# Kernel tuning notes

Hardware: AMD Instinct MI355X
Metric: run time of the kernel (lower is better)

The kernel has to match this reference:

```python
import jax, jax.numpy as jnp
import numpy as np

N_NODES = 50000
N_EDGES = 800000
D = 128
RRELU_SLOPE = (1.0 / 8.0 + 1.0 / 3.0) / 2.0  # eval-mode RReLU = leaky relu with mean slope 11/48


def setup_inputs() -> dict:
    key = jax.random.key(0)
    ks = jax.random.split(key, 10)
    s = 1.0 / np.sqrt(D)
    return {
        "node_feats": jax.random.normal(ks[0], (N_NODES, D), dtype=jnp.float32),
        "edge_feats": jax.random.normal(ks[1], (N_EDGES, D), dtype=jnp.float32),
        "src": jax.random.randint(ks[2], (N_EDGES,), 0, N_NODES, dtype=jnp.int32),
        "dst": jax.random.randint(ks[3], (N_EDGES,), 0, N_NODES, dtype=jnp.int32),
        "Wn0": jax.random.uniform(ks[4], (D, D), jnp.float32, -s, s),
        "Ws0": jax.random.uniform(ks[5], (D, D), jnp.float32, -s, s),
        "Wi0": jax.random.uniform(ks[6], (D, D), jnp.float32, -s, s),
        "Wn1": jax.random.uniform(ks[7], (D, D), jnp.float32, -s, s),
        "Ws1": jax.random.uniform(ks[8], (D, D), jnp.float32, -s, s),
        "Wi1": jax.random.uniform(ks[9], (D, D), jnp.float32, -s, s),
    }


def _layer(h, edge_feats, src, dst, deg, iso, Wn, Ws, Wi, num_nodes):
    # per-edge message: neigh_linear(src_h + edge_h)
    msg = (h[src] + edge_feats) @ Wn.T  # [E, H]
    # mean aggregate to destination; nodes with no in-edges get 0 (DGL semantics)
    agg = jax.ops.segment_sum(msg, dst, num_segments=num_nodes)
    agg = agg / jnp.maximum(deg, 1.0)[:, None]
    # self-loop message, replaced by isolated-node message where in_degree == 0
    self_msg = jnp.where(iso[:, None], h @ Wi.T, h @ Ws.T)
    x = agg + self_msg
    # RReLU in eval mode = leaky relu with slope (lower+upper)/2
    return jnp.where(x >= 0, x, RRELU_SLOPE * x)


def reference(node_feats, edge_feats, src, dst, Wn0, Ws0, Wi0, Wn1, Ws1, Wi1):
    num_nodes = node_feats.shape[0]
    deg = jax.ops.segment_sum(
        jnp.ones(src.shape[0], dtype=node_feats.dtype), dst, num_segments=num_nodes
    )
    iso = deg == 0
    h = _layer(node_feats, edge_feats, src, dst, deg, iso, Wn0, Ws0, Wi0, num_nodes)
    h = _layer(h, edge_feats, src, dst, deg, iso, Wn1, Ws1, Wi1, num_nodes)
    return h
```

## Files before the change

### kernel.cpp

```cpp
#include <hip/hip_runtime.h>
#include <hip/hip_bf16.h>

#define N_NODES 50000
#define N_EDGES 800000
#define D 128
#define D2 64

static constexpr float SLOPE = 11.0f / 48.0f;

typedef __attribute__((ext_vector_type(8))) short bf16x8;
typedef __attribute__((ext_vector_type(4))) float f32x4;
typedef __attribute__((ext_vector_type(2))) unsigned int u32x2;
typedef __attribute__((ext_vector_type(4))) unsigned int u32x4;

__device__ __forceinline__ float bf_lo(unsigned int v) { return __uint_as_float(v << 16); }
__device__ __forceinline__ float bf_hi(unsigned int v) { return __uint_as_float(v & 0xffff0000u); }

__device__ __forceinline__ unsigned short f2bf(float x) {
    __hip_bfloat16 b = __float2bfloat16(x);
    return *(unsigned short*)&b;
}

__device__ __forceinline__ unsigned int pack_bf2(float lo, float hi) {
    return ((unsigned int)f2bf(hi) << 16) | (unsigned int)f2bf(lo);
}


__global__ void k_cvt_nf(const f32x4* __restrict__ in, u32x4* __restrict__ out) {
    int i = blockIdx.x * 256 + threadIdx.x;
    if (i >= N_NODES * D / 8) return;
    f32x4 lo = in[2 * i];
    f32x4 hi = in[2 * i + 1];
    u32x4 o;
    o.x = pack_bf2(lo[0], lo[1]);
    o.y = pack_bf2(lo[2], lo[3]);
    o.z = pack_bf2(hi[0], hi[1]);
    o.w = pack_bf2(hi[2], hi[3]);
    out[i] = o;
}

__global__ void k_cvt_w(const float* __restrict__ Wn0, const float* __restrict__ Ws0,
                        const float* __restrict__ Wn1, const float* __restrict__ Ws1,
                        unsigned int* __restrict__ out) {
    int i = blockIdx.x * 256 + threadIdx.x;
    int m = i >> 11;
    int j = i & 2047;
    const float* W = (m == 0) ? Wn0 : (m == 1) ? Ws0 : (m == 2) ? Wn1 : Ws1;
    f32x4 lo = ((const f32x4*)W)[2 * j];
    f32x4 hi = ((const f32x4*)W)[2 * j + 1];
    u32x4 o;
    o.x = pack_bf2(lo[0], lo[1]);
    o.y = pack_bf2(lo[2], lo[3]);
    o.z = pack_bf2(hi[0], hi[1]);
    o.w = pack_bf2(hi[2], hi[3]);
    *(u32x4*)(out + (size_t)m * 8192 + 4 * j) = o;
}


__global__ void k_count(const int* __restrict__ dst, int* __restrict__ deg) {
    int e = blockIdx.x * 256 + threadIdx.x;
    if (e < N_EDGES) atomicAdd(&deg[dst[e]], 1);
}

__global__ void k_scan1(const int* __restrict__ deg, int* __restrict__ offs,
                        int* __restrict__ part) {
    __shared__ int sm[256];
    int t = threadIdx.x;
    int i = blockIdx.x * 256 + t;
    int v = (i < N_NODES) ? deg[i] : 0;
    int orig = v;
    sm[t] = v;
    __syncthreads();
    for (int off = 1; off < 256; off <<= 1) {
        int x = (t >= off) ? sm[t - off] : 0;
        __syncthreads();
        sm[t] += x;
        __syncthreads();
    }
    if (i < N_NODES) offs[i] = sm[t] - orig;
    if (t == 255) part[blockIdx.x] = sm[t];
}

__global__ void k_scan2(int* __restrict__ part, int nb) {
    __shared__ int sm[256];
    int t = threadIdx.x;
    int v = (t < nb) ? part[t] : 0;
    int orig = v;
    sm[t] = v;
    __syncthreads();
    for (int off = 1; off < 256; off <<= 1) {
        int x = (t >= off) ? sm[t - off] : 0;
        __syncthreads();
        sm[t] += x;
        __syncthreads();
    }
    if (t < nb) part[t] = sm[t] - orig;
}

__global__ void k_scan3(int* __restrict__ offs, const int* __restrict__ part) {
    int i = blockIdx.x * 256 + threadIdx.x;
    if (i < N_NODES) offs[i] += part[blockIdx.x];
}

__global__ void k_fill(const int* __restrict__ src, const int* __restrict__ dst,
                       const int* __restrict__ offs, int* __restrict__ cur,
                       int2* __restrict__ csr) {
    int e = blockIdx.x * 256 + threadIdx.x;
    if (e < N_EDGES) {
        int d = dst[e];
        int p = offs[d] + atomicAdd(&cur[d], 1);
        csr[p] = make_int2(src[e], e);
    }
}

__global__ void k_iso(const int* __restrict__ deg, int* __restrict__ isolist,
                      int* __restrict__ niso) {
    int i = blockIdx.x * 256 + threadIdx.x;
    if (i < N_NODES && deg[i] == 0) {
        int p = atomicAdd(niso, 1);
        isolist[p] = i;
    }
}


__global__ void k_agg_ef(const unsigned int* __restrict__ nfb,
                         const f32x4* __restrict__ ef,
                         const int2* __restrict__ csr,
                         const int* __restrict__ offs, const int* __restrict__ deg,
                         unsigned int* __restrict__ efsum,
                         unsigned int* __restrict__ pre) {
    int node = blockIdx.x * 4 + (threadIdx.x >> 6);
    if (node >= N_NODES) return;
    int lane = threadIdx.x & 63;
    int half = lane >> 5;
    int c = lane & 31;
    int start = offs[node];
    int cnt = deg[node];
    f32x4 ae = {0.f, 0.f, 0.f, 0.f};
    f32x4 ah = {0.f, 0.f, 0.f, 0.f};
#pragma unroll 2
    for (int k = half; k < cnt; k += 2) {
        int2 se = csr[start + k];
        f32x4 ev = ef[(size_t)se.y * 32 + c];
        u32x2 hv = *(const u32x2*)(nfb + (size_t)se.x * D2 + 2 * c);
        ae[0] += ev[0];
        ae[1] += ev[1];
        ae[2] += ev[2];
        ae[3] += ev[3];
        ah[0] += bf_lo(hv.x);
        ah[1] += bf_hi(hv.x);
        ah[2] += bf_lo(hv.y);
        ah[3] += bf_hi(hv.y);
    }
#pragma unroll
    for (int i = 0; i < 4; ++i) {
        ae[i] += __shfl_xor(ae[i], 32);
        ah[i] += __shfl_xor(ah[i], 32);
    }
    float inv = 1.0f / fmaxf((float)cnt, 1.0f);
    if (half == 0) {
        u32x2 eo;
        eo.x = pack_bf2(ae[0], ae[1]);
        eo.y = pack_bf2(ae[2], ae[3]);
        *(u32x2*)(efsum + (size_t)node * D2 + 2 * c) = eo;
    } else {
        u32x2 po;
        po.x = pack_bf2((ah[0] + ae[0]) * inv, (ah[1] + ae[1]) * inv);
        po.y = pack_bf2((ah[2] + ae[2]) * inv, (ah[3] + ae[3]) * inv);
        *(u32x2*)(pre + (size_t)node * D2 + 2 * c) = po;
    }
}


__global__ void k_agg2(const unsigned int* __restrict__ h,
                       const int2* __restrict__ csr,
                       const int* __restrict__ offs, const int* __restrict__ deg,
                       const unsigned int* __restrict__ efsum,
                       unsigned int* __restrict__ pre) {
    int node = blockIdx.x * 4 + (threadIdx.x >> 6);
    if (node >= N_NODES) return;
    int lane = threadIdx.x & 63;
    int q = lane >> 4;
    int g = lane & 15;
    int start = offs[node];
    int cnt = deg[node];
    float a[8] = {0.f, 0.f, 0.f, 0.f, 0.f, 0.f, 0.f, 0.f};
#pragma unroll 2
    for (int k = q; k < cnt; k += 4) {
        int2 se = csr[start + k];
        u32x4 hv = *(const u32x4*)(h + (size_t)se.x * D2 + 4 * g);
        a[0] += bf_lo(hv.x);
        a[1] += bf_hi(hv.x);
        a[2] += bf_lo(hv.y);
        a[3] += bf_hi(hv.y);
        a[4] += bf_lo(hv.z);
        a[5] += bf_hi(hv.z);
        a[6] += bf_lo(hv.w);
        a[7] += bf_hi(hv.w);
    }
#pragma unroll
    for (int i = 0; i < 8; ++i) {
        a[i] += __shfl_xor(a[i], 16);
        a[i] += __shfl_xor(a[i], 32);
    }
    if (q == 0) {
        u32x4 es = *(const u32x4*)(efsum + (size_t)node * D2 + 4 * g);
        float inv = 1.0f / fmaxf((float)cnt, 1.0f);
        float r0 = (a[0] + bf_lo(es.x)) * inv;
        float r1 = (a[1] + bf_hi(es.x)) * inv;
        float r2 = (a[2] + bf_lo(es.y)) * inv;
        float r3 = (a[3] + bf_hi(es.y)) * inv;
        float r4 = (a[4] + bf_lo(es.z)) * inv;
        float r5 = (a[5] + bf_hi(es.z)) * inv;
        float r6 = (a[6] + bf_lo(es.w)) * inv;
        float r7 = (a[7] + bf_hi(es.w)) * inv;
        u32x4 o;
        o.x = pack_bf2(r0, r1);
        o.y = pack_bf2(r2, r3);
        o.z = pack_bf2(r4, r5);
        o.w = pack_bf2(r6, r7);
        *(u32x4*)(pre + (size_t)node * D2 + 4 * g) = o;
    }
}


template <int OUT_F32>
__global__ void k_gemm(const unsigned short* __restrict__ A1,
                       const unsigned short* __restrict__ A2,
                       const unsigned short* __restrict__ W1,
                       const unsigned short* __restrict__ W2,
                       void* __restrict__ outv) {
    int wave = threadIdx.x >> 6;
    int lane = threadIdx.x & 63;
    int quad = lane >> 4;
    int r16 = lane & 15;
    int m0 = (blockIdx.x * 4 + wave) * 32;

    f32x4 acc[2][8];
#pragma unroll
    for (int mt = 0; mt < 2; ++mt)
#pragma unroll
        for (int nt = 0; nt < 8; ++nt) acc[mt][nt] = (f32x4){0.f, 0.f, 0.f, 0.f};

    int rowA0 = min(m0 + r16, N_NODES - 1);
    int rowA1 = min(m0 + 16 + r16, N_NODES - 1);

#pragma unroll
    for (int ks = 0; ks < 8; ++ks) {
        int koff = (ks & 3) * 32 + quad * 8;
        const unsigned short* Asrc = (ks < 4) ? A1 : A2;
        bf16x8 a0 = *(const bf16x8*)(Asrc + (size_t)rowA0 * D + koff);
        bf16x8 a1 = *(const bf16x8*)(Asrc + (size_t)rowA1 * D + koff);
        const unsigned short* Wsrc = (ks < 4) ? W1 : W2;
#pragma unroll
        for (int nt = 0; nt < 8; ++nt) {
            bf16x8 b = *(const bf16x8*)(Wsrc + (size_t)(nt * 16 + r16) * D + koff);
            acc[0][nt] = __builtin_amdgcn_mfma_f32_16x16x32_bf16(a0, b, acc[0][nt], 0, 0, 0);
            acc[1][nt] = __builtin_amdgcn_mfma_f32_16x16x32_bf16(a1, b, acc[1][nt], 0, 0, 0);
        }
    }

#pragma unroll
    for (int mt = 0; mt < 2; ++mt) {
#pragma unroll
        for (int r = 0; r < 4; ++r) {
            int row = m0 + mt * 16 + quad * 4 + r;
            if (row < N_NODES) {
#pragma unroll
                for (int nt = 0; nt < 8; ++nt) {
                    float x = acc[mt][nt][r];
                    x = (x >= 0.f) ? x : x * SLOPE;
                    if (OUT_F32)
                        ((float*)outv)[(size_t)row * D + nt * 16 + r16] = x;
                    else
                        ((unsigned short*)outv)[(size_t)row * D + nt * 16 + r16] = f2bf(x);
                }
            }
        }
    }
}


__global__ void k_fixup1(const unsigned int* __restrict__ nfb,
                         const float* __restrict__ Wi,
                         const int* __restrict__ isolist, const int* __restrict__ niso,
                         unsigned short* __restrict__ out) {
    int w = blockIdx.x * 4 + (threadIdx.x >> 6);
    int lane = threadIdx.x & 63;
    int n = *niso;
    for (int t = w; t < n; t += gridDim.x * 4) {
        int node = isolist[t];
        const unsigned int* hrow = nfb + (size_t)node * D2;
        float a0 = 0.f, a1 = 0.f;
        for (int ku = 0; ku < D2; ++ku) {
            unsigned int v = hrow[ku];
            float h0 = bf_lo(v), h1 = bf_hi(v);
            a0 += h0 * Wi[(size_t)lane * D + 2 * ku] + h1 * Wi[(size_t)lane * D + 2 * ku + 1];
            a1 += h0 * Wi[(size_t)(lane + 64) * D + 2 * ku] +
                  h1 * Wi[(size_t)(lane + 64) * D + 2 * ku + 1];
        }
        a0 = (a0 >= 0.f) ? a0 : a0 * SLOPE;
        a1 = (a1 >= 0.f) ? a1 : a1 * SLOPE;
        out[(size_t)node * D + lane] = f2bf(a0);
        out[(size_t)node * D + lane + 64] = f2bf(a1);
    }
}

__global__ void k_fixup2(const unsigned short* __restrict__ h,
                         const float* __restrict__ Wi,
                         const int* __restrict__ isolist, const int* __restrict__ niso,
                         float* __restrict__ out) {
    int w = blockIdx.x * 4 + (threadIdx.x >> 6);
    int lane = threadIdx.x & 63;
    int n = *niso;
    for (int t = w; t < n; t += gridDim.x * 4) {
        int node = isolist[t];
        const unsigned short* hrow = h + (size_t)node * D;
        float a0 = 0.f, a1 = 0.f;
        for (int k = 0; k < D; ++k) {
            float hk = __uint_as_float(((unsigned int)hrow[k]) << 16);
            a0 += hk * Wi[(size_t)lane * D + k];
            a1 += hk * Wi[(size_t)(lane + 64) * D + k];
        }
        a0 = (a0 >= 0.f) ? a0 : a0 * SLOPE;
        a1 = (a1 >= 0.f) ? a1 : a1 * SLOPE;
        out[(size_t)node * D + lane] = a0;
        out[(size_t)node * D + lane + 64] = a1;
    }
}


extern "C" void kernel_launch(void* const* d_in, const int* in_sizes, int n_in,
                              void* d_out, int out_size, void* d_ws, size_t ws_size,
                              hipStream_t stream) {
    const float* node_feats = (const float*)d_in[0];
    const float* edge_feats = (const float*)d_in[1];
    const int* src = (const int*)d_in[2];
    const int* dst = (const int*)d_in[3];
    const float* Wn0 = (const float*)d_in[4];
    const float* Ws0 = (const float*)d_in[5];
    const float* Wi0 = (const float*)d_in[6];
    const float* Wn1 = (const float*)d_in[7];
    const float* Ws1 = (const float*)d_in[8];
    const float* Wi1 = (const float*)d_in[9];

    char* ws = (char*)d_ws;
    size_t o = 0;
    auto alloc = [&](size_t bytes) -> char* {
        char* p = ws + o;
        o += (bytes + 255) & ~size_t(255);
        return p;
    };
    int* deg = (int*)alloc((size_t)N_NODES * 4);
    int* cur = (int*)alloc((size_t)N_NODES * 4);
    int* niso = (int*)alloc(256);
    int* offs = (int*)alloc((size_t)N_NODES * 4);
    int* part = (int*)alloc(1024);
    int* isolist = (int*)alloc((size_t)N_NODES * 4);
    int2* csr = (int2*)alloc((size_t)N_EDGES * 8);
    unsigned int* efsum = (unsigned int*)alloc((size_t)N_NODES * D * 2);
    unsigned int* pre = (unsigned int*)alloc((size_t)N_NODES * D * 2);
    unsigned int* h1 = (unsigned int*)alloc((size_t)N_NODES * D * 2);
    unsigned int* nfb = (unsigned int*)alloc((size_t)N_NODES * D * 2);
    unsigned int* wbf = (unsigned int*)alloc(4 * 8192 * 4);

    hipMemsetAsync(deg, 0, 2 * (((size_t)N_NODES * 4 + 255) & ~size_t(255)) + 256, stream);

    int ebl = (N_EDGES + 255) / 256;
    int nbl = (N_NODES + 255) / 256;
    int nwb = (N_NODES + 3) / 4;
    int gbl = (N_NODES + 127) / 128;

    k_cvt_nf<<<(N_NODES * D / 8 + 255) / 256, 256, 0, stream>>>((const f32x4*)node_feats,
                                                                (u32x4*)nfb);
    k_cvt_w<<<32, 256, 0, stream>>>(Wn0, Ws0, Wn1, Ws1, wbf);
    k_count<<<ebl, 256, 0, stream>>>(dst, deg);
    k_scan1<<<nbl, 256, 0, stream>>>(deg, offs, part);
    k_scan2<<<1, 256, 0, stream>>>(part, nbl);
    k_scan3<<<nbl, 256, 0, stream>>>(offs, part);
    k_fill<<<ebl, 256, 0, stream>>>(src, dst, offs, cur, csr);
    k_iso<<<nbl, 256, 0, stream>>>(deg, isolist, niso);

    const unsigned short* Wn0b = (const unsigned short*)(wbf + 0 * 8192);
    const unsigned short* Ws0b = (const unsigned short*)(wbf + 1 * 8192);
    const unsigned short* Wn1b = (const unsigned short*)(wbf + 2 * 8192);
    const unsigned short* Ws1b = (const unsigned short*)(wbf + 3 * 8192);

    k_agg_ef<<<nwb, 256, 0, stream>>>(nfb, (const f32x4*)edge_feats, csr, offs, deg, efsum, pre);
    k_gemm<0><<<gbl, 256, 0, stream>>>((const unsigned short*)pre, (const unsigned short*)nfb,
                                       Wn0b, Ws0b, (void*)h1);
    k_fixup1<<<32, 256, 0, stream>>>(nfb, Wi0, isolist, niso, (unsigned short*)h1);

    k_agg2<<<nwb, 256, 0, stream>>>(h1, csr, offs, deg, efsum, pre);
    k_gemm<1><<<gbl, 256, 0, stream>>>((const unsigned short*)pre, (const unsigned short*)h1,
                                       Wn1b, Ws1b, d_out);
    k_fixup2<<<32, 256, 0, stream>>>((const unsigned short*)h1, Wi1, isolist, niso, (float*)d_out);
}
```

Measured before the change: 757.0 us.

## Merge setup kernels, widen gather lanes, and halve GEMM wave tile

Merges the node-feature and weight conversions into one launch and folds the isolated-node list building into the first scan kernel. The scan now writes absolute offsets into the cursor array, so the fill kernel no longer reads offs and the memset shrinks. The edge-aggregation kernels are regrouped so each lane issues wider vector loads over more edges at once (4 and 8 edges in parallel per wave). The GEMM drops from 32 to 16 rows per wave and doubles the block count, trading B-fragment reuse for more parallelism.

```diff
diff --git a/kernel.cpp b/kernel.cpp
--- a/kernel.cpp
+++ b/kernel.cpp
@@ -26,34 +26,37 @@
 }
 
 
-__global__ void k_cvt_nf(const f32x4* __restrict__ in, u32x4* __restrict__ out) {
+__global__ void k_cvt(const f32x4* __restrict__ nf, const float* __restrict__ Wn0,
+                      const float* __restrict__ Ws0, const float* __restrict__ Wn1,
+                      const float* __restrict__ Ws1, u32x4* __restrict__ nfb,
+                      unsigned int* __restrict__ wbf) {
     int i = blockIdx.x * 256 + threadIdx.x;
-    if (i >= N_NODES * D / 8) return;
-    f32x4 lo = in[2 * i];
-    f32x4 hi = in[2 * i + 1];
-    u32x4 o;
-    o.x = pack_bf2(lo[0], lo[1]);
-    o.y = pack_bf2(lo[2], lo[3]);
-    o.z = pack_bf2(hi[0], hi[1]);
-    o.w = pack_bf2(hi[2], hi[3]);
-    out[i] = o;
-}
-
-__global__ void k_cvt_w(const float* __restrict__ Wn0, const float* __restrict__ Ws0,
-                        const float* __restrict__ Wn1, const float* __restrict__ Ws1,
-                        unsigned int* __restrict__ out) {
-    int i = blockIdx.x * 256 + threadIdx.x;
-    int m = i >> 11;
-    int j = i & 2047;
-    const float* W = (m == 0) ? Wn0 : (m == 1) ? Ws0 : (m == 2) ? Wn1 : Ws1;
-    f32x4 lo = ((const f32x4*)W)[2 * j];
-    f32x4 hi = ((const f32x4*)W)[2 * j + 1];
-    u32x4 o;
-    o.x = pack_bf2(lo[0], lo[1]);
-    o.y = pack_bf2(lo[2], lo[3]);
-    o.z = pack_bf2(hi[0], hi[1]);
-    o.w = pack_bf2(hi[2], hi[3]);
-    *(u32x4*)(out + (size_t)m * 8192 + 4 * j) = o;
+    const int NNF = N_NODES * D / 8;
+    if (i < NNF) {
+        f32x4 lo = nf[2 * i];
+        f32x4 hi = nf[2 * i + 1];
+        u32x4 o;
+        o.x = pack_bf2(lo[0], lo[1]);
+        o.y = pack_bf2(lo[2], lo[3]);
+        o.z = pack_bf2(hi[0], hi[1]);
+        o.w = pack_bf2(hi[2], hi[3]);
+        nfb[i] = o;
+    } else {
+        int j = i - NNF;
+        if (j < 8192) {
+            int m = j >> 11;
+            int t = j & 2047;
+            const float* W = (m == 0) ? Wn0 : (m == 1) ? Ws0 : (m == 2) ? Wn1 : Ws1;
+            f32x4 lo = ((const f32x4*)W)[2 * t];
+            f32x4 hi = ((const f32x4*)W)[2 * t + 1];
+            u32x4 o;
+            o.x = pack_bf2(lo[0], lo[1]);
+            o.y = pack_bf2(lo[2], lo[3]);
+            o.z = pack_bf2(hi[0], hi[1]);
+            o.w = pack_bf2(hi[2], hi[3]);
+            *(u32x4*)(wbf + (size_t)m * 8192 + 4 * t) = o;
+        }
+    }
 }
 
 
@@ -63,12 +66,17 @@
 }
 
 __global__ void k_scan1(const int* __restrict__ deg, int* __restrict__ offs,
-                        int* __restrict__ part) {
+                        int* __restrict__ part, int* __restrict__ isolist,
+                        int* __restrict__ niso) {
     __shared__ int sm[256];
     int t = threadIdx.x;
     int i = blockIdx.x * 256 + t;
     int v = (i < N_NODES) ? deg[i] : 0;
     int orig = v;
+    if (i < N_NODES && orig == 0) {
+        int p = atomicAdd(niso, 1);
+        isolist[p] = i;
+    }
     sm[t] = v;
     __syncthreads();
     for (int off = 1; off < 256; off <<= 1) {
@@ -97,28 +105,22 @@
     if (t < nb) part[t] = sm[t] - orig;
 }
 
-__global__ void k_scan3(int* __restrict__ offs, const int* __restrict__ part) {
+__global__ void k_scan3(int* __restrict__ offs, const int* __restrict__ part,
+                        int* __restrict__ cur) {
     int i = blockIdx.x * 256 + threadIdx.x;
-    if (i < N_NODES) offs[i] += part[blockIdx.x];
+    if (i < N_NODES) {
+        int v = offs[i] + part[blockIdx.x];
+        offs[i] = v;
+        cur[i] = v;
+    }
 }
 
 __global__ void k_fill(const int* __restrict__ src, const int* __restrict__ dst,
-                       const int* __restrict__ offs, int* __restrict__ cur,
-                       int2* __restrict__ csr) {
+                       int* __restrict__ cur, int2* __restrict__ csr) {
     int e = blockIdx.x * 256 + threadIdx.x;
     if (e < N_EDGES) {
-        int d = dst[e];
-        int p = offs[d] + atomicAdd(&cur[d], 1);
+        int p = atomicAdd(&cur[dst[e]], 1);
         csr[p] = make_int2(src[e], e);
-    }
-}
-
-__global__ void k_iso(const int* __restrict__ deg, int* __restrict__ isolist,
-                      int* __restrict__ niso) {
-    int i = blockIdx.x * 256 + threadIdx.x;
-    if (i < N_NODES && deg[i] == 0) {
-        int p = atomicAdd(niso, 1);
-        isolist[p] = i;
     }
 }
 
@@ -132,42 +134,57 @@
     int node = blockIdx.x * 4 + (threadIdx.x >> 6);
     if (node >= N_NODES) return;
     int lane = threadIdx.x & 63;
-    int half = lane >> 5;
-    int c = lane & 31;
+    int q = lane >> 4;
+    int g = lane & 15;
     int start = offs[node];
     int cnt = deg[node];
-    f32x4 ae = {0.f, 0.f, 0.f, 0.f};
-    f32x4 ah = {0.f, 0.f, 0.f, 0.f};
+    float ae[8] = {0.f, 0.f, 0.f, 0.f, 0.f, 0.f, 0.f, 0.f};
+    float ah[8] = {0.f, 0.f, 0.f, 0.f, 0.f, 0.f, 0.f, 0.f};
 #pragma unroll 2
-    for (int k = half; k < cnt; k += 2) {
+    for (int k = q; k < cnt; k += 4) {
         int2 se = csr[start + k];
-        f32x4 ev = ef[(size_t)se.y * 32 + c];
-        u32x2 hv = *(const u32x2*)(nfb + (size_t)se.x * D2 + 2 * c);
-        ae[0] += ev[0];
-        ae[1] += ev[1];
-        ae[2] += ev[2];
-        ae[3] += ev[3];
+        f32x4 e0 = ef[(size_t)se.y * 32 + 2 * g];
+        f32x4 e1 = ef[(size_t)se.y * 32 + 2 * g + 1];
+        u32x4 hv = *(const u32x4*)(nfb + (size_t)se.x * D2 + 4 * g);
+        ae[0] += e0[0];
+        ae[1] += e0[1];
+        ae[2] += e0[2];
+        ae[3] += e0[3];
+        ae[4] += e1[0];
+        ae[5] += e1[1];
+        ae[6] += e1[2];
+        ae[7] += e1[3];
         ah[0] += bf_lo(hv.x);
         ah[1] += bf_hi(hv.x);
         ah[2] += bf_lo(hv.y);
         ah[3] += bf_hi(hv.y);
-    }
-#pragma unroll
-    for (int i = 0; i < 4; ++i) {
+        ah[4] += bf_lo(hv.z);
+        ah[5] += bf_hi(hv.z);
+        ah[6] += bf_lo(hv.w);
+        ah[7] += bf_hi(hv.w);
+    }
+#pragma unroll
+    for (int i = 0; i < 8; ++i) {
+        ae[i] += __shfl_xor(ae[i], 16);
         ae[i] += __shfl_xor(ae[i], 32);
+        ah[i] += __shfl_xor(ah[i], 16);
         ah[i] += __shfl_xor(ah[i], 32);
     }
     float inv = 1.0f / fmaxf((float)cnt, 1.0f);
-    if (half == 0) {
-        u32x2 eo;
+    if (q == 0) {
+        u32x4 eo;
         eo.x = pack_bf2(ae[0], ae[1]);
         eo.y = pack_bf2(ae[2], ae[3]);
-        *(u32x2*)(efsum + (size_t)node * D2 + 2 * c) = eo;
-    } else {
-        u32x2 po;
+        eo.z = pack_bf2(ae[4], ae[5]);
+        eo.w = pack_bf2(ae[6], ae[7]);
+        *(u32x4*)(efsum + (size_t)node * D2 + 4 * g) = eo;
+    } else if (q == 1) {
+        u32x4 po;
         po.x = pack_bf2((ah[0] + ae[0]) * inv, (ah[1] + ae[1]) * inv);
         po.y = pack_bf2((ah[2] + ae[2]) * inv, (ah[3] + ae[3]) * inv);
-        *(u32x2*)(pre + (size_t)node * D2 + 2 * c) = po;
+        po.z = pack_bf2((ah[4] + ae[4]) * inv, (ah[5] + ae[5]) * inv);
+        po.w = pack_bf2((ah[6] + ae[6]) * inv, (ah[7] + ae[7]) * inv);
+        *(u32x4*)(pre + (size_t)node * D2 + 4 * g) = po;
     }
 }
 
@@ -180,46 +197,56 @@
     int node = blockIdx.x * 4 + (threadIdx.x >> 6);
     if (node >= N_NODES) return;
     int lane = threadIdx.x & 63;
-    int q = lane >> 4;
-    int g = lane & 15;
+    int e = lane >> 3;
+    int g = lane & 7;
     int start = offs[node];
     int cnt = deg[node];
-    float a[8] = {0.f, 0.f, 0.f, 0.f, 0.f, 0.f, 0.f, 0.f};
+    float a[16];
+#pragma unroll
+    for (int i = 0; i < 16; ++i) a[i] = 0.f;
 #pragma unroll 2
-    for (int k = q; k < cnt; k += 4) {
+    for (int k = e; k < cnt; k += 8) {
         int2 se = csr[start + k];
-        u32x4 hv = *(const u32x4*)(h + (size_t)se.x * D2 + 4 * g);
-        a[0] += bf_lo(hv.x);
-        a[1] += bf_hi(hv.x);
-        a[2] += bf_lo(hv.y);
-        a[3] += bf_hi(hv.y);
-        a[4] += bf_lo(hv.z);
-        a[5] += bf_hi(hv.z);
-        a[6] += bf_lo(hv.w);
-        a[7] += bf_hi(hv.w);
-    }
-#pragma unroll
-    for (int i = 0; i < 8; ++i) {
+        u32x4 h0 = *(const u32x4*)(h + (size_t)se.x * D2 + 8 * g);
+        u32x4 h1v = *(const u32x4*)(h + (size_t)se.x * D2 + 8 * g + 4);
+        a[0] += bf_lo(h0.x);
+        a[1] += bf_hi(h0.x);
+        a[2] += bf_lo(h0.y);
+        a[3] += bf_hi(h0.y);
+        a[4] += bf_lo(h0.z);
+        a[5] += bf_hi(h0.z);
+        a[6] += bf_lo(h0.w);
+        a[7] += bf_hi(h0.w);
+        a[8] += bf_lo(h1v.x);
+        a[9] += bf_hi(h1v.x);
+        a[10] += bf_lo(h1v.y);
+        a[11] += bf_hi(h1v.y);
+        a[12] += bf_lo(h1v.z);
+        a[13] += bf_hi(h1v.z);
+        a[14] += bf_lo(h1v.w);
+        a[15] += bf_hi(h1v.w);
+    }
+#pragma unroll
+    for (int i = 0; i < 16; ++i) {
+        a[i] += __shfl_xor(a[i], 8);
         a[i] += __shfl_xor(a[i], 16);
         a[i] += __shfl_xor(a[i], 32);
     }
-    if (q == 0) {
-        u32x4 es = *(const u32x4*)(efsum + (size_t)node * D2 + 4 * g);
+    if (e == 0) {
+        u32x4 e0 = *(const u32x4*)(efsum + (size_t)node * D2 + 8 * g);
+        u32x4 e1 = *(const u32x4*)(efsum + (size_t)node * D2 + 8 * g + 4);
         float inv = 1.0f / fmaxf((float)cnt, 1.0f);
-        float r0 = (a[0] + bf_lo(es.x)) * inv;
-        float r1 = (a[1] + bf_hi(es.x)) * inv;
-        float r2 = (a[2] + bf_lo(es.y)) * inv;
-        float r3 = (a[3] + bf_hi(es.y)) * inv;
-        float r4 = (a[4] + bf_lo(es.z)) * inv;
-        float r5 = (a[5] + bf_hi(es.z)) * inv;
-        float r6 = (a[6] + bf_lo(es.w)) * inv;
-        float r7 = (a[7] + bf_hi(es.w)) * inv;
-        u32x4 o;
-        o.x = pack_bf2(r0, r1);
-        o.y = pack_bf2(r2, r3);
-        o.z = pack_bf2(r4, r5);
-        o.w = pack_bf2(r6, r7);
-        *(u32x4*)(pre + (size_t)node * D2 + 4 * g) = o;
+        u32x4 o0, o1;
+        o0.x = pack_bf2((a[0] + bf_lo(e0.x)) * inv, (a[1] + bf_hi(e0.x)) * inv);
+        o0.y = pack_bf2((a[2] + bf_lo(e0.y)) * inv, (a[3] + bf_hi(e0.y)) * inv);
+        o0.z = pack_bf2((a[4] + bf_lo(e0.z)) * inv, (a[5] + bf_hi(e0.z)) * inv);
+        o0.w = pack_bf2((a[6] + bf_lo(e0.w)) * inv, (a[7] + bf_hi(e0.w)) * inv);
+        o1.x = pack_bf2((a[8] + bf_lo(e1.x)) * inv, (a[9] + bf_hi(e1.x)) * inv);
+        o1.y = pack_bf2((a[10] + bf_lo(e1.y)) * inv, (a[11] + bf_hi(e1.y)) * inv);
+        o1.z = pack_bf2((a[12] + bf_lo(e1.z)) * inv, (a[13] + bf_hi(e1.z)) * inv);
+        o1.w = pack_bf2((a[14] + bf_lo(e1.w)) * inv, (a[15] + bf_hi(e1.w)) * inv);
+        *(u32x4*)(pre + (size_t)node * D2 + 8 * g) = o0;
+        *(u32x4*)(pre + (size_t)node * D2 + 8 * g + 4) = o1;
     }
 }
 
@@ -234,47 +261,39 @@
     int lane = threadIdx.x & 63;
     int quad = lane >> 4;
     int r16 = lane & 15;
-    int m0 = (blockIdx.x * 4 + wave) * 32;
-
-    f32x4 acc[2][8];
-#pragma unroll
-    for (int mt = 0; mt < 2; ++mt)
-#pragma unroll
-        for (int nt = 0; nt < 8; ++nt) acc[mt][nt] = (f32x4){0.f, 0.f, 0.f, 0.f};
-
-    int rowA0 = min(m0 + r16, N_NODES - 1);
-    int rowA1 = min(m0 + 16 + r16, N_NODES - 1);
+    int m0 = (blockIdx.x * 4 + wave) * 16;
+
+    f32x4 acc[8];
+#pragma unroll
+    for (int nt = 0; nt < 8; ++nt) acc[nt] = (f32x4){0.f, 0.f, 0.f, 0.f};
+
+    int rowA = min(m0 + r16, N_NODES - 1);
 
 #pragma unroll
     for (int ks = 0; ks < 8; ++ks) {
         int koff = (ks & 3) * 32 + quad * 8;
         const unsigned short* Asrc = (ks < 4) ? A1 : A2;
-        bf16x8 a0 = *(const bf16x8*)(Asrc + (size_t)rowA0 * D + koff);
-        bf16x8 a1 = *(const bf16x8*)(Asrc + (size_t)rowA1 * D + koff);
+        bf16x8 a = *(const bf16x8*)(Asrc + (size_t)rowA * D + koff);
         const unsigned short* Wsrc = (ks < 4) ? W1 : W2;
 #pragma unroll
         for (int nt = 0; nt < 8; ++nt) {
             bf16x8 b = *(const bf16x8*)(Wsrc + (size_t)(nt * 16 + r16) * D + koff);
-            acc[0][nt] = __builtin_amdgcn_mfma_f32_16x16x32_bf16(a0, b, acc[0][nt], 0, 0, 0);
-            acc[1][nt] = __builtin_amdgcn_mfma_f32_16x16x32_bf16(a1, b, acc[1][nt], 0, 0, 0);
+            acc[nt] = __builtin_amdgcn_mfma_f32_16x16x32_bf16(a, b, acc[nt], 0, 0, 0);
         }
     }
 
 #pragma unroll
-    for (int mt = 0; mt < 2; ++mt) {
-#pragma unroll
-        for (int r = 0; r < 4; ++r) {
-            int row = m0 + mt * 16 + quad * 4 + r;
-            if (row < N_NODES) {
-#pragma unroll
-                for (int nt = 0; nt < 8; ++nt) {
-                    float x = acc[mt][nt][r];
-                    x = (x >= 0.f) ? x : x * SLOPE;
-                    if (OUT_F32)
-                        ((float*)outv)[(size_t)row * D + nt * 16 + r16] = x;
-                    else
-                        ((unsigned short*)outv)[(size_t)row * D + nt * 16 + r16] = f2bf(x);
-                }
+    for (int r = 0; r < 4; ++r) {
+        int row = m0 + quad * 4 + r;
+        if (row < N_NODES) {
+#pragma unroll
+            for (int nt = 0; nt < 8; ++nt) {
+                float x = acc[nt][r];
+                x = (x >= 0.f) ? x : x * SLOPE;
+                if (OUT_F32)
+                    ((float*)outv)[(size_t)row * D + nt * 16 + r16] = x;
+                else
+                    ((unsigned short*)outv)[(size_t)row * D + nt * 16 + r16] = f2bf(x);
             }
         }
     }
@@ -352,8 +371,8 @@
         return p;
     };
     int* deg = (int*)alloc((size_t)N_NODES * 4);
+    int* niso = (int*)alloc(256);
     int* cur = (int*)alloc((size_t)N_NODES * 4);
-    int* niso = (int*)alloc(256);
     int* offs = (int*)alloc((size_t)N_NODES * 4);
     int* part = (int*)alloc(1024);
     int* isolist = (int*)alloc((size_t)N_NODES * 4);
@@ -364,22 +383,21 @@
     unsigned int* nfb = (unsigned int*)alloc((size_t)N_NODES * D * 2);
     unsigned int* wbf = (unsigned int*)alloc(4 * 8192 * 4);
 
-    hipMemsetAsync(deg, 0, 2 * (((size_t)N_NODES * 4 + 255) & ~size_t(255)) + 256, stream);
+    hipMemsetAsync(deg, 0, (((size_t)N_NODES * 4 + 255) & ~size_t(255)) + 256, stream);
 
     int ebl = (N_EDGES + 255) / 256;
     int nbl = (N_NODES + 255) / 256;
     int nwb = (N_NODES + 3) / 4;
-    int gbl = (N_NODES + 127) / 128;
-
-    k_cvt_nf<<<(N_NODES * D / 8 + 255) / 256, 256, 0, stream>>>((const f32x4*)node_feats,
-                                                                (u32x4*)nfb);
-    k_cvt_w<<<32, 256, 0, stream>>>(Wn0, Ws0, Wn1, Ws1, wbf);
+    int gbl = (N_NODES + 63) / 64;
+    int cbl = (N_NODES * D / 8 + 8192 + 255) / 256;
+
+    k_cvt<<<cbl, 256, 0, stream>>>((const f32x4*)node_feats, Wn0, Ws0, Wn1, Ws1,
+                                   (u32x4*)nfb, wbf);
     k_count<<<ebl, 256, 0, stream>>>(dst, deg);
-    k_scan1<<<nbl, 256, 0, stream>>>(deg, offs, part);
+    k_scan1<<<nbl, 256, 0, stream>>>(deg, offs, part, isolist, niso);
     k_scan2<<<1, 256, 0, stream>>>(part, nbl);
-    k_scan3<<<nbl, 256, 0, stream>>>(offs, part);
-    k_fill<<<ebl, 256, 0, stream>>>(src, dst, offs, cur, csr);
-    k_iso<<<nbl, 256, 0, stream>>>(deg, isolist, niso);
+    k_scan3<<<nbl, 256, 0, stream>>>(offs, part, cur);
+    k_fill<<<ebl, 256, 0, stream>>>(src, dst, cur, csr);
 
     const unsigned short* Wn0b = (const unsigned short*)(wbf + 0 * 8192);
     const unsigned short* Ws0b = (const unsigned short*)(wbf + 1 * 8192);
```

Result: slower. 782.6 us (+3.4%).
